# Kernel tuning notes

Measured on AMD Instinct MI355X. Metric: run time of the kernel, lower is better.

The kernel has to match this reference:

```python
import jax, jax.numpy as jnp
import numpy as np

N, E, F_IN = 100000, 3200000, 512
H1, D1, C = 8, 8, 16  # layer1 heads, per-head dim; layer2 out classes
NEG_SLOPE = 0.2


def _segment_softmax(e, dst, num_segments):
    # numerically-stable softmax over edges grouped by destination node
    m = jax.ops.segment_max(e, dst, num_segments=num_segments)
    ex = jnp.exp(e - m[dst])
    s = jax.ops.segment_sum(ex, dst, num_segments=num_segments)
    return ex / (s[dst] + 1e-16)


def _gat_layer(x, src, dst, W, a_src, a_dst, heads, d_out):
    n = x.shape[0]
    h = (x @ W).reshape(n, heads, d_out)          # [N,H,D]
    al_s = jnp.einsum('nhd,hd->nh', h, a_src)     # [N,H]
    al_d = jnp.einsum('nhd,hd->nh', h, a_dst)
    e = jax.nn.leaky_relu(al_s[src] + al_d[dst], NEG_SLOPE)  # [E,H]
    alpha = _segment_softmax(e, dst, n)           # [E,H]
    msg = h[src] * alpha[..., None]               # [E,H,D]
    return jax.ops.segment_sum(msg, dst, num_segments=n)  # [N,H,D]


def setup_inputs() -> dict:
    key = jax.random.key(0)
    ks = jax.random.split(key, 8)
    x = jax.random.normal(ks[0], (N, F_IN), dtype=jnp.float32)
    edge_index = jax.random.randint(ks[1], (2, E), 0, N, dtype=jnp.int64)
    W1 = jax.random.normal(ks[2], (F_IN, H1 * D1), dtype=jnp.float32) * (1.0 / np.sqrt(F_IN))
    a1_src = jax.random.normal(ks[3], (H1, D1), dtype=jnp.float32)
    a1_dst = jax.random.normal(ks[4], (H1, D1), dtype=jnp.float32)
    W2 = jax.random.normal(ks[5], (H1 * D1, C), dtype=jnp.float32) * (1.0 / np.sqrt(H1 * D1))
    a2_src = jax.random.normal(ks[6], (1, C), dtype=jnp.float32)
    a2_dst = jax.random.normal(ks[7], (1, C), dtype=jnp.float32)
    return {'x': x, 'edge_index': edge_index, 'W1': W1, 'a1_src': a1_src,
            'a1_dst': a1_dst, 'W2': W2, 'a2_src': a2_src, 'a2_dst': a2_dst}


def reference(x, edge_index, W1, a1_src, a1_dst, W2, a2_src, a2_dst):
    src, dst = edge_index[0], edge_index[1]
    # layer 1: 8 heads, concat, then ELU (dropout is identity in eval mode)
    h1 = _gat_layer(x, src, dst, W1, a1_src, a1_dst, H1, D1)  # [N,H1,D1]
    h1 = jax.nn.elu(h1.reshape(N, H1 * D1))                   # [N,64]
    # layer 2: single head -> class logits
    h2 = _gat_layer(h1, src, dst, W2, a2_src, a2_dst, 1, C)   # [N,1,C]
    return jax.nn.log_softmax(h2.reshape(N, C), axis=1)
```

## Files before the change

### kernel.cpp

```cpp
#include <hip/hip_runtime.h>
#include <math.h>

#define NEG 0.2f
#define NB 64
#define BCAP 128
#define WS 544

typedef __attribute__((ext_vector_type(8))) short bf16x8;
typedef __attribute__((ext_vector_type(4))) float f32x4;
typedef unsigned long long ull;

#define GL4(dst, ptr) asm volatile("global_load_dwordx4 %0, %1, off" : "=v"(dst) : "v"(ptr))

static __device__ __forceinline__ float lrelu(float x){ return x > 0.f ? x : NEG*x; }

static __device__ __forceinline__ void bsplit(float v, unsigned int& hi, unsigned int& lo){
  unsigned int u = __float_as_uint(v);
  unsigned int hb = (u + 0x7fffu + ((u >> 16) & 1u)) & 0xffff0000u;
  float hf = __uint_as_float(hb);
  float l = v - hf;
  unsigned int ul = __float_as_uint(l);
  hi = hb >> 16;
  lo = (ul + 0x7fffu + ((ul >> 16) & 1u)) >> 16;
}

static __device__ __forceinline__ float bf2f(unsigned short u){
  return __uint_as_float(((unsigned int)u) << 16);
}
static __device__ __forceinline__ unsigned short f2bf(float v){
  unsigned int u = __float_as_uint(v);
  return (unsigned short)((u + 0x7fffu + ((u >> 16) & 1u)) >> 16);
}

static __device__ __forceinline__ bf16x8 cvt8(f32x4 v0, f32x4 v1){
  bf16x8 r;
  #pragma unroll
  for (int i = 0; i < 4; ++i) r[i] = (short)f2bf(v0[i]);
  #pragma unroll
  for (int i = 0; i < 4; ++i) r[4+i] = (short)f2bf(v1[i]);
  return r;
}

__global__ void k_prep(const int* __restrict__ u, int* __restrict__ flag,
                       int* __restrict__ pcur, const float* __restrict__ W1,
                       unsigned short* __restrict__ wtH, unsigned short* __restrict__ wtL){
  int t = blockIdx.x*256 + threadIdx.x;
  if (t < NB*8*16) pcur[t] = 0;
  else if (t < NB*8*16 + 512*64) {
    int i = t - NB*8*16;
    int c = i & 63;
    unsigned int hi, lo;
    bsplit(W1[i], hi, lo);
    wtH[c*WS + (i >> 6)] = (unsigned short)hi;
    wtL[c*WS + (i >> 6)] = (unsigned short)lo;
  } else if (t == NB*8*16 + 512*64) {
    int z = 1;
    for (int e = 0; e < 64; ++e) if (u[2*e+1] != 0) { z = 0; break; }
    *flag = z;
  }
}

__global__ __launch_bounds__(256) void k_part(const int* __restrict__ u,
    const int* __restrict__ flag, int* __restrict__ pcur,
    ull* __restrict__ part, int E, int n, int SEGCAP){
  __shared__ ull buf[NB][BCAP];
  __shared__ int bcnt[NB];
  __shared__ int binc[NB];
  __shared__ int bbase;
  __shared__ int nflush;
  __shared__ unsigned char flist[NB];
  const bool f = (*flag) != 0;
  const int tid = threadIdx.x;
  const int g = blockIdx.x & 7;
  if (tid < NB) bcnt[tid] = 0;
  const long long stride = (long long)gridDim.x * 256;
  const long long iters = ((long long)E + stride - 1) / stride;
  long long e = (long long)blockIdx.x*256 + tid;
  for (long long it = 0; it < iters; ++it, e += stride) {
    if (tid < NB) binc[tid] = 0;
    if (tid == 0) nflush = 0;
    __syncthreads();
    int src = 0, dst = 0, b = 0;
    const bool valid = (e < E);
    if (valid) {
      src = f ? u[2*e] : u[e];
      dst = f ? u[2*(E+e)] : u[E+e];
      b = (int)(((long long)dst * NB) / n);
      atomicAdd(&binc[b], 1);
    }
    __syncthreads();
    if (tid < NB && bcnt[tid] > 0 && bcnt[tid] + binc[tid] > BCAP) {
      int i = atomicAdd(&nflush, 1);
      flist[i] = (unsigned char)tid;
    }
    __syncthreads();
    for (int i = 0; i < nflush; ++i) {
      int b2 = flist[i];
      int c = bcnt[b2]; if (c > BCAP) c = BCAP;
      if (tid == 0) bbase = atomicAdd(&pcur[(b2*8+g)*16], c);
      __syncthreads();
      int base = bbase;
      for (int j = tid; j < c; j += 256) {
        int pos = base + j;
        if (pos < SEGCAP) part[(size_t)(b2*8+g)*SEGCAP + pos] = buf[b2][j];
      }
      __syncthreads();
      if (tid == 0) bcnt[b2] = 0;
      __syncthreads();
    }
    if (valid) {
      int pos = atomicAdd(&bcnt[b], 1);
      if (pos < BCAP) buf[b][pos] = (ull)(unsigned)src | ((ull)(unsigned)dst << 32);
    }
    __syncthreads();
  }
  for (int b2 = 0; b2 < NB; ++b2) {
    int c = bcnt[b2]; if (c > BCAP) c = BCAP;
    if (c > 0) {
      if (tid == 0) bbase = atomicAdd(&pcur[(b2*8+g)*16], c);
      __syncthreads();
      int base = bbase;
      for (int j = tid; j < c; j += 256) {
        int pos = base + j;
        if (pos < SEGCAP) part[(size_t)(b2*8+g)*SEGCAP + pos] = buf[b2][j];
      }
    }
    __syncthreads();
  }
}

__global__ __launch_bounds__(1024) void k_histL(const int* __restrict__ pcur,
    const ull* __restrict__ part, int* __restrict__ cnt, int n, int SEGCAP){
  __shared__ int lcnt[1664];
  const int b = blockIdx.x;
  const int lo = (int)(((long long)b * n + NB - 1) / NB);
  const int hi = (int)(((long long)(b+1) * n + NB - 1) / NB);
  const int m = hi - lo;
  for (int i = threadIdx.x; i < m; i += 1024) lcnt[i] = 0;
  __syncthreads();
  for (int g = 0; g < 8; ++g) {
    int s = b*8 + g;
    int c = pcur[s*16]; if (c > SEGCAP) c = SEGCAP;
    for (int i = threadIdx.x; i < c; i += 1024) {
      ull v = __builtin_nontemporal_load(&part[(size_t)s*SEGCAP + i]);
      atomicAdd(&lcnt[(int)(unsigned)(v >> 32) - lo], 1);
    }
  }
  __syncthreads();
  for (int i = threadIdx.x; i < m; i += 1024) cnt[lo + i] = lcnt[i];
}

__global__ __launch_bounds__(256) void k_scan1(const int* __restrict__ cnt,
    int* __restrict__ ro, int* __restrict__ bsum, int n){
  int t = threadIdx.x;
  int base = blockIdx.x*1024 + t*4;
  int v0 = (base+0 < n) ? cnt[base+0] : 0;
  int v1 = (base+1 < n) ? cnt[base+1] : 0;
  int v2 = (base+2 < n) ? cnt[base+2] : 0;
  int v3 = (base+3 < n) ? cnt[base+3] : 0;
  int s = v0+v1+v2+v3;
  int lane = t & 63, w = t >> 6;
  int inc = s;
  for (int off = 1; off < 64; off <<= 1) {
    int tm = __shfl_up(inc, off);
    if (lane >= off) inc += tm;
  }
  __shared__ int wsum[4];
  if (lane == 63) wsum[w] = inc;
  __syncthreads();
  int wpre = 0;
  for (int k = 0; k < 4; ++k) if (k < w) wpre += wsum[k];
  int run = wpre + inc - s;
  if (base+0 < n) ro[base+0] = run; run += v0;
  if (base+1 < n) ro[base+1] = run; run += v1;
  if (base+2 < n) ro[base+2] = run; run += v2;
  if (base+3 < n) ro[base+3] = run; run += v3;
  if (t == 255) bsum[blockIdx.x] = run;
}

__global__ void k_scan2(int* __restrict__ bsum, int nb){
  int lane = threadIdx.x;
  int carry = 0;
  for (int b = 0; b < nb; b += 64) {
    int i = b + lane;
    int v = (i < nb) ? bsum[i] : 0;
    int inc = v;
    for (int off = 1; off < 64; off <<= 1) {
      int t = __shfl_up(inc, off);
      if (lane >= off) inc += t;
    }
    if (i < nb) bsum[i] = carry + inc - v;
    carry += __shfl(inc, 63);
  }
}

__global__ void k_scan3(int* __restrict__ ro, const int* __restrict__ bsum,
                        int* __restrict__ csr, int n, int E){
  int i = blockIdx.x*blockDim.x + threadIdx.x;
  if (i < n) ro[i] = ro[i] + bsum[i >> 10];
  if (i == 0) ro[n] = E;
  if (i < 16) csr[E + i] = 0;
}

__global__ __launch_bounds__(1024) void k_fillL(const int* __restrict__ pcur,
    const ull* __restrict__ part, const int* __restrict__ ro,
    int* __restrict__ csr, int n, int SEGCAP){
  __shared__ int lcur[1664];
  const int b = blockIdx.x;
  const int lo = (int)(((long long)b * n + NB - 1) / NB);
  const int hi = (int)(((long long)(b+1) * n + NB - 1) / NB);
  const int m = hi - lo;
  for (int i = threadIdx.x; i < m; i += 1024) lcur[i] = ro[lo + i];
  __syncthreads();
  for (int g = 0; g < 8; ++g) {
    int s = b*8 + g;
    int c = pcur[s*16]; if (c > SEGCAP) c = SEGCAP;
    for (int i = threadIdx.x; i < c; i += 1024) {
      ull v = __builtin_nontemporal_load(&part[(size_t)s*SEGCAP + i]);
      int src = (int)(unsigned)v;
      int dst = (int)(unsigned)(v >> 32);
      int p = atomicAdd(&lcur[dst - lo], 1);
      csr[p] = src;
    }
  }
}

__global__ __launch_bounds__(256, 3) void k_proj1(const float* __restrict__ x,
    const unsigned short* __restrict__ wtH, const unsigned short* __restrict__ wtL,
    const float* __restrict__ a1s_g, const float* __restrict__ a1d_g,
    unsigned short* __restrict__ h1bf, float* __restrict__ al1s, float* __restrict__ al1d, int n){
  const int tid = threadIdx.x;
  const int lane = tid & 63;
  const int w = tid >> 6;
  const int l16 = lane & 15;
  const int lhi = lane >> 4;
  const int r0 = blockIdx.x*128 + w*32;

  float as_c[4], ad_c[4];
  #pragma unroll
  for (int f = 0; f < 4; ++f) { as_c[f] = a1s_g[16*f + l16]; ad_c[f] = a1d_g[16*f + l16]; }

  f32x4 acc[2][4];
  #pragma unroll
  for (int m = 0; m < 2; ++m)
    #pragma unroll
    for (int f = 0; f < 4; ++f) acc[m][f] = (f32x4){0.f,0.f,0.f,0.f};

  int rowA = r0 + l16;        if (rowA >= n) rowA = n - 1;
  int rowB = r0 + 16 + l16;   if (rowB >= n) rowB = n - 1;
  const float* xA = x + (size_t)rowA*512 + 8*lhi;
  const float* xB = x + (size_t)rowB*512 + 8*lhi;
  const unsigned short* wHp = wtH + (size_t)l16*WS + 8*lhi;
  const unsigned short* wLp = wtL + (size_t)l16*WS + 8*lhi;

  for (int k0 = 0; k0 < 512; k0 += 64) {
    f32x4 a0, a1v, a2, a3, b0, b1v, b2, b3;
    bf16x8 bh0[4], bl0[4], bh1[4], bl1[4];
    GL4(a0,  xA + k0);      GL4(a1v, xA + k0 + 4);
    GL4(a2,  xA + k0 + 32); GL4(a3,  xA + k0 + 36);
    GL4(b0,  xB + k0);      GL4(b1v, xB + k0 + 4);
    GL4(b2,  xB + k0 + 32); GL4(b3,  xB + k0 + 36);
    #pragma unroll
    for (int f = 0; f < 4; ++f) {
      GL4(bh0[f], wHp + (size_t)f*16*WS + k0);
      GL4(bl0[f], wLp + (size_t)f*16*WS + k0);
      GL4(bh1[f], wHp + (size_t)f*16*WS + k0 + 32);
      GL4(bl1[f], wLp + (size_t)f*16*WS + k0 + 32);
    }
    asm volatile("s_waitcnt vmcnt(0)" ::: "memory");
    __builtin_amdgcn_sched_barrier(0);
    bf16x8 ahA0 = cvt8(a0, a1v), ahA1 = cvt8(a2, a3);
    bf16x8 ahB0 = cvt8(b0, b1v), ahB1 = cvt8(b2, b3);
    #pragma unroll
    for (int f = 0; f < 4; ++f) {
      acc[0][f] = __builtin_amdgcn_mfma_f32_16x16x32_bf16(ahA0, bh0[f], acc[0][f], 0, 0, 0);
      acc[0][f] = __builtin_amdgcn_mfma_f32_16x16x32_bf16(ahA0, bl0[f], acc[0][f], 0, 0, 0);
      acc[0][f] = __builtin_amdgcn_mfma_f32_16x16x32_bf16(ahA1, bh1[f], acc[0][f], 0, 0, 0);
      acc[0][f] = __builtin_amdgcn_mfma_f32_16x16x32_bf16(ahA1, bl1[f], acc[0][f], 0, 0, 0);
      acc[1][f] = __builtin_amdgcn_mfma_f32_16x16x32_bf16(ahB0, bh0[f], acc[1][f], 0, 0, 0);
      acc[1][f] = __builtin_amdgcn_mfma_f32_16x16x32_bf16(ahB0, bl0[f], acc[1][f], 0, 0, 0);
      acc[1][f] = __builtin_amdgcn_mfma_f32_16x16x32_bf16(ahB1, bh1[f], acc[1][f], 0, 0, 0);
      acc[1][f] = __builtin_amdgcn_mfma_f32_16x16x32_bf16(ahB1, bl1[f], acc[1][f], 0, 0, 0);
    }
  }

  #pragma unroll
  for (int m = 0; m < 2; ++m) {
    #pragma unroll
    for (int r = 0; r < 4; ++r) {
      int node = r0 + 16*m + 4*lhi + r;
      bool ok = (node < n);
      #pragma unroll
      for (int f = 0; f < 4; ++f) {
        float v = acc[m][f][r];
        if (ok) h1bf[(size_t)node*64 + 16*f + l16] = f2bf(v);
        float vs = v * as_c[f], vd = v * ad_c[f];
        vs += __shfl_xor(vs, 1); vs += __shfl_xor(vs, 2); vs += __shfl_xor(vs, 4);
        vd += __shfl_xor(vd, 1); vd += __shfl_xor(vd, 2); vd += __shfl_xor(vd, 4);
        if (ok && (l16 & 7) == 0) {
          int head = 2*f + (l16 >> 3);
          al1s[node*8 + head] = vs;
          al1d[node*8 + head] = vd;
        }
      }
    }
  }
}

__global__ __launch_bounds__(256) void k_agg1(const int* __restrict__ ro,
    const int* __restrict__ csr, const float* __restrict__ al1s,
    const float* __restrict__ al1d, const unsigned short* __restrict__ h1bf,
    float* __restrict__ h1b, int n){
  int wid = blockIdx.x*4 + (threadIdx.x >> 6);
  if (wid >= n) return;
  int node = __builtin_amdgcn_readfirstlane(wid);
  int lane = threadIdx.x & 63;
  int half = lane >> 5;
  int sl = lane & 31;
  int h = sl >> 2;
  int beg = ro[node], end = ro[node+1];
  float ald = al1d[node*8 + h];
  float s = 0.f, accA = 0.f, accB = 0.f;
  if (beg < end) {
    int srcb[4]; float alb[4]; unsigned hvb[4];
    #pragma unroll
    for (int j = 0; j < 4; ++j) srcb[j] = csr[beg + 2*j + half];
    #pragma unroll
    for (int j = 0; j < 4; ++j) {
      alb[j] = al1s[srcb[j]*8 + h];
      hvb[j] = *(const unsigned*)&h1bf[(size_t)srcb[j]*64 + 2*sl];
    }
    for (int t = beg; t < end; t += 8) {
      int nsrc[4]; float nal[4]; unsigned nhv[4];
      #pragma unroll
      for (int j = 0; j < 4; ++j) nsrc[j] = csr[t + 8 + 2*j + half];
      #pragma unroll
      for (int j = 0; j < 4; ++j) {
        nal[j] = al1s[nsrc[j]*8 + h];
        nhv[j] = *(const unsigned*)&h1bf[(size_t)nsrc[j]*64 + 2*sl];
      }
      #pragma unroll
      for (int j = 0; j < 4; ++j) {
        float e = alb[j] + ald;
        e = e > 0.f ? e : NEG*e;
        float ex = (t + 2*j + half < end) ? __expf(e) : 0.f;
        s += ex;
        unsigned u = hvb[j];
        accA = fmaf(__uint_as_float(u << 16), ex, accA);
        accB = fmaf(__uint_as_float(u & 0xffff0000u), ex, accB);
      }
      #pragma unroll
      for (int j = 0; j < 4; ++j) { srcb[j] = nsrc[j]; alb[j] = nal[j]; hvb[j] = nhv[j]; }
    }
  }
  s    += __shfl_xor(s, 32);
  accA += __shfl_xor(accA, 32);
  accB += __shfl_xor(accB, 32);
  if (half == 0) {
    float inv = 1.f / (s + 1e-16f);
    float vA = accA * inv, vB = accB * inv;
    vA = vA > 0.f ? vA : expm1f(vA);
    vB = vB > 0.f ? vB : expm1f(vB);
    *(float2*)&h1b[(size_t)node*64 + 2*sl] = make_float2(vA, vB);
  }
}

__global__ __launch_bounds__(256) void k_proj2(const float* __restrict__ h1b,
    const float* __restrict__ W2, const float* __restrict__ a2s_g, const float* __restrict__ a2d_g,
    unsigned short* __restrict__ h2bf, float* __restrict__ al2s, float* __restrict__ al2d, int n){
  __shared__ float w[64*16];
  __shared__ float a2sv[16], a2dv[16];
  for (int i = threadIdx.x; i < 1024; i += 256) w[i] = W2[i];
  if (threadIdx.x < 16) { a2sv[threadIdx.x] = a2s_g[threadIdx.x]; a2dv[threadIdx.x] = a2d_g[threadIdx.x]; }
  __syncthreads();
  int c = threadIdx.x & 15;
  int nid = blockIdx.x*16 + (threadIdx.x >> 4);
  if (nid >= n) return;
  const float* row = h1b + (size_t)nid*64;
  float acc = 0.f;
  #pragma unroll
  for (int k0 = 0; k0 < 64; k0 += 4) {
    float4 r = *(const float4*)(row + k0);
    acc = fmaf(r.x, w[(k0+0)*16 + c], acc);
    acc = fmaf(r.y, w[(k0+1)*16 + c], acc);
    acc = fmaf(r.z, w[(k0+2)*16 + c], acc);
    acc = fmaf(r.w, w[(k0+3)*16 + c], acc);
  }
  h2bf[(size_t)nid*16 + c] = f2bf(acc);
  float vs = acc * a2sv[c], vd = acc * a2dv[c];
  vs += __shfl_xor(vs, 1); vs += __shfl_xor(vs, 2); vs += __shfl_xor(vs, 4); vs += __shfl_xor(vs, 8);
  vd += __shfl_xor(vd, 1); vd += __shfl_xor(vd, 2); vd += __shfl_xor(vd, 4); vd += __shfl_xor(vd, 8);
  if (c == 0) { al2s[nid] = vs; al2d[nid] = vd; }
}

__global__ __launch_bounds__(256) void k_agg2(const int* __restrict__ ro,
    const int* __restrict__ csr, const float* __restrict__ al2s,
    const float* __restrict__ al2d, const unsigned short* __restrict__ h2bf,
    float* __restrict__ out, int n){
  int wid = blockIdx.x*4 + (threadIdx.x >> 6);
  if (wid >= n) return;
  int node = __builtin_amdgcn_readfirstlane(wid);
  int lane = threadIdx.x & 63;
  int j = lane >> 4, c = lane & 15;
  int beg = ro[node], end = ro[node+1];
  float ald = al2d[node];
  float sp = 0.f, acc = 0.f;
  if (beg < end) {
    int iA = beg + j;
    int sA = csr[iA];
    int sB = csr[iA + 4];
    float aA = al2s[sA];
    float hA = bf2f(h2bf[(size_t)sA*16 + c]);
    float aB = al2s[sB];
    float hB = bf2f(h2bf[(size_t)sB*16 + c]);
    for (int i = iA; i < end; i += 4) {
      int sC = csr[i + 8];
      float aC = al2s[sC];
      float hC = bf2f(h2bf[(size_t)sC*16 + c]);
      float e = lrelu(aA + ald);
      float ex = __expf(e);
      sp += ex;
      acc = fmaf(ex, hA, acc);
      aA = aB; hA = hB; aB = aC; hB = hC;
    }
  }
  sp  += __shfl_xor(sp, 16);  sp  += __shfl_xor(sp, 32);
  acc += __shfl_xor(acc, 16); acc += __shfl_xor(acc, 32);
  float v = acc / (sp + 1e-16f);
  float mx = v;
  mx = fmaxf(mx, __shfl_xor(mx, 1)); mx = fmaxf(mx, __shfl_xor(mx, 2));
  mx = fmaxf(mx, __shfl_xor(mx, 4)); mx = fmaxf(mx, __shfl_xor(mx, 8));
  float l = v - mx;
  float se = __expf(l);
  se += __shfl_xor(se, 1); se += __shfl_xor(se, 2);
  se += __shfl_xor(se, 4); se += __shfl_xor(se, 8);
  float res = l - logf(se);
  if (j == 0) out[(size_t)node*16 + c] = res;
}

static inline size_t alignup(size_t x){ return (x + 255) & ~(size_t)255; }

extern "C" void kernel_launch(void* const* d_in, const int* in_sizes, int n_in,
                              void* d_out, int out_size, void* d_ws, size_t ws_size,
                              hipStream_t stream){
  const float* x   = (const float*)d_in[0];
  const int*   ei  = (const int*)  d_in[1];
  const float* W1  = (const float*)d_in[2];
  const float* a1s = (const float*)d_in[3];
  const float* a1d = (const float*)d_in[4];
  const float* W2  = (const float*)d_in[5];
  const float* a2s = (const float*)d_in[6];
  const float* a2d = (const float*)d_in[7];
  float* out = (float*)d_out;

  const int n = in_sizes[0] / 512;
  const int E = in_sizes[1] / 2;

  char* w = (char*)d_ws;
  unsigned short* h1bf = (unsigned short*)w; w += alignup((size_t)n*64*2);
  float* h1b  = (float*)w; w += alignup((size_t)n*64*4);
  float* al1s_ = (float*)w; w += alignup((size_t)n*8*4);
  float* al1d_ = (float*)w; w += alignup((size_t)n*8*4);
  unsigned short* h2bf = (unsigned short*)w; w += alignup((size_t)n*16*2);
  float* al2s_ = (float*)w; w += alignup((size_t)n*4);
  float* al2d_ = (float*)w; w += alignup((size_t)n*4);
  int* cnt    = (int*)w;   w += alignup((size_t)n*4);
  int* ro     = (int*)w;   w += alignup((size_t)(n+1)*4);
  int* csr    = (int*)w;   w += alignup((size_t)(E+16)*4);
  int* bsum   = (int*)w;   w += alignup(512*4);
  int* flag   = (int*)w;   w += alignup(64);
  int* pcur   = (int*)w;   w += alignup((size_t)NB*8*16*4);
  unsigned short* wtH = (unsigned short*)w; w += alignup((size_t)64*WS*2);
  unsigned short* wtL = (unsigned short*)w; w += alignup((size_t)64*WS*2);

  ull* part = (ull*)h1bf;
  const int SEGCAP = 9300;

  const int nb_scan = (n + 1023) / 1024;
  const int prep_threads = NB*8*16 + 512*64 + 1;

  k_prep<<<(prep_threads + 255)/256, 256, 0, stream>>>(ei, flag, pcur, W1, wtH, wtL);
  k_part<<<1024, 256, 0, stream>>>(ei, flag, pcur, part, E, n, SEGCAP);
  k_histL<<<NB, 1024, 0, stream>>>(pcur, part, cnt, n, SEGCAP);
  k_scan1<<<nb_scan, 256, 0, stream>>>(cnt, ro, bsum, n);
  k_scan2<<<1, 64, 0, stream>>>(bsum, nb_scan);
  k_scan3<<<(n+255)/256, 256, 0, stream>>>(ro, bsum, csr, n, E);
  k_fillL<<<NB, 1024, 0, stream>>>(pcur, part, ro, csr, n, SEGCAP);

  k_proj1<<<(n+127)/128, 256, 0, stream>>>(x, wtH, wtL, a1s, a1d, h1bf, al1s_, al1d_, n);
  k_agg1<<<(n+3)/4, 256, 0, stream>>>(ro, csr, al1s_, al1d_, h1bf, h1b, n);
  k_proj2<<<(n+15)/16, 256, 0, stream>>>(h1b, W2, a2s, a2d, h2bf, al2s_, al2d_, n);
  k_agg2<<<(n+3)/4, 256, 0, stream>>>(ro, csr, al2s_, al2d_, h2bf, out, n);
}
```

Baseline: 484.5 us.

## Fuse edge partitioning and layer-1 projection into one concurrent kernel launch

Merges the edge bucketing kernel and the layer-1 MFMA projection into a single launch, with the first 1024 blocks partitioning edges and the rest computing x@W1. Partitioning is atomic/latency bound and the projection streams x through the MFMA units, so running them side by side is meant to overlap the two phases and drop one launch. The partition buffer no longer aliases h1bf, so it gets its own ~38MB of workspace. Launch bounds drop to 2 blocks/CU because of the shared-memory buffer, which may reduce occupancy for the projection blocks.

```diff
diff --git a/kernel.cpp b/kernel.cpp
--- a/kernel.cpp
+++ b/kernel.cpp
@@ -5,6 +5,7 @@
 #define NB 64
 #define BCAP 128
 #define WS 544
+#define NPART 1024
 
 typedef __attribute__((ext_vector_type(8))) short bf16x8;
 typedef __attribute__((ext_vector_type(4))) float f32x4;
@@ -60,72 +61,157 @@
   }
 }
 
-__global__ __launch_bounds__(256) void k_part(const int* __restrict__ u,
-    const int* __restrict__ flag, int* __restrict__ pcur,
-    ull* __restrict__ part, int E, int n, int SEGCAP){
+__global__ __launch_bounds__(256, 2) void k_p1p(
+    const int* __restrict__ u, const int* __restrict__ flag,
+    int* __restrict__ pcur, ull* __restrict__ part, int E, int n, int SEGCAP,
+    const float* __restrict__ x,
+    const unsigned short* __restrict__ wtH, const unsigned short* __restrict__ wtL,
+    const float* __restrict__ a1s_g, const float* __restrict__ a1d_g,
+    unsigned short* __restrict__ h1bf, float* __restrict__ al1s, float* __restrict__ al1d){
   __shared__ ull buf[NB][BCAP];
   __shared__ int bcnt[NB];
   __shared__ int binc[NB];
   __shared__ int bbase;
   __shared__ int nflush;
   __shared__ unsigned char flist[NB];
-  const bool f = (*flag) != 0;
+
+  if (blockIdx.x < NPART) {
+    const bool f = (*flag) != 0;
+    const int tid = threadIdx.x;
+    const int g = blockIdx.x & 7;
+    if (tid < NB) bcnt[tid] = 0;
+    const long long stride = (long long)NPART * 256;
+    const long long iters = ((long long)E + stride - 1) / stride;
+    long long e = (long long)blockIdx.x*256 + tid;
+    for (long long it = 0; it < iters; ++it, e += stride) {
+      if (tid < NB) binc[tid] = 0;
+      if (tid == 0) nflush = 0;
+      __syncthreads();
+      int src = 0, dst = 0, b = 0;
+      const bool valid = (e < E);
+      if (valid) {
+        src = f ? u[2*e] : u[e];
+        dst = f ? u[2*(E+e)] : u[E+e];
+        b = (int)(((long long)dst * NB) / n);
+        atomicAdd(&binc[b], 1);
+      }
+      __syncthreads();
+      if (tid < NB && bcnt[tid] > 0 && bcnt[tid] + binc[tid] > BCAP) {
+        int i = atomicAdd(&nflush, 1);
+        flist[i] = (unsigned char)tid;
+      }
+      __syncthreads();
+      for (int i = 0; i < nflush; ++i) {
+        int b2 = flist[i];
+        int c = bcnt[b2]; if (c > BCAP) c = BCAP;
+        if (tid == 0) bbase = atomicAdd(&pcur[(b2*8+g)*16], c);
+        __syncthreads();
+        int base = bbase;
+        for (int j = tid; j < c; j += 256) {
+          int pos = base + j;
+          if (pos < SEGCAP) part[(size_t)(b2*8+g)*SEGCAP + pos] = buf[b2][j];
+        }
+        __syncthreads();
+        if (tid == 0) bcnt[b2] = 0;
+        __syncthreads();
+      }
+      if (valid) {
+        int pos = atomicAdd(&bcnt[b], 1);
+        if (pos < BCAP) buf[b][pos] = (ull)(unsigned)src | ((ull)(unsigned)dst << 32);
+      }
+      __syncthreads();
+    }
+    for (int b2 = 0; b2 < NB; ++b2) {
+      int c = bcnt[b2]; if (c > BCAP) c = BCAP;
+      if (c > 0) {
+        if (tid == 0) bbase = atomicAdd(&pcur[(b2*8+g)*16], c);
+        __syncthreads();
+        int base = bbase;
+        for (int j = tid; j < c; j += 256) {
+          int pos = base + j;
+          if (pos < SEGCAP) part[(size_t)(b2*8+g)*SEGCAP + pos] = buf[b2][j];
+        }
+      }
+      __syncthreads();
+    }
+    return;
+  }
+
   const int tid = threadIdx.x;
-  const int g = blockIdx.x & 7;
-  if (tid < NB) bcnt[tid] = 0;
-  const long long stride = (long long)gridDim.x * 256;
-  const long long iters = ((long long)E + stride - 1) / stride;
-  long long e = (long long)blockIdx.x*256 + tid;
-  for (long long it = 0; it < iters; ++it, e += stride) {
-    if (tid < NB) binc[tid] = 0;
-    if (tid == 0) nflush = 0;
-    __syncthreads();
-    int src = 0, dst = 0, b = 0;
-    const bool valid = (e < E);
-    if (valid) {
-      src = f ? u[2*e] : u[e];
-      dst = f ? u[2*(E+e)] : u[E+e];
-      b = (int)(((long long)dst * NB) / n);
-      atomicAdd(&binc[b], 1);
-    }
-    __syncthreads();
-    if (tid < NB && bcnt[tid] > 0 && bcnt[tid] + binc[tid] > BCAP) {
-      int i = atomicAdd(&nflush, 1);
-      flist[i] = (unsigned char)tid;
-    }
-    __syncthreads();
-    for (int i = 0; i < nflush; ++i) {
-      int b2 = flist[i];
-      int c = bcnt[b2]; if (c > BCAP) c = BCAP;
-      if (tid == 0) bbase = atomicAdd(&pcur[(b2*8+g)*16], c);
-      __syncthreads();
-      int base = bbase;
-      for (int j = tid; j < c; j += 256) {
-        int pos = base + j;
-        if (pos < SEGCAP) part[(size_t)(b2*8+g)*SEGCAP + pos] = buf[b2][j];
-      }
-      __syncthreads();
-      if (tid == 0) bcnt[b2] = 0;
-      __syncthreads();
-    }
-    if (valid) {
-      int pos = atomicAdd(&bcnt[b], 1);
-      if (pos < BCAP) buf[b][pos] = (ull)(unsigned)src | ((ull)(unsigned)dst << 32);
-    }
-    __syncthreads();
-  }
-  for (int b2 = 0; b2 < NB; ++b2) {
-    int c = bcnt[b2]; if (c > BCAP) c = BCAP;
-    if (c > 0) {
-      if (tid == 0) bbase = atomicAdd(&pcur[(b2*8+g)*16], c);
-      __syncthreads();
-      int base = bbase;
-      for (int j = tid; j < c; j += 256) {
-        int pos = base + j;
-        if (pos < SEGCAP) part[(size_t)(b2*8+g)*SEGCAP + pos] = buf[b2][j];
-      }
-    }
-    __syncthreads();
+  const int lane = tid & 63;
+  const int w = tid >> 6;
+  const int l16 = lane & 15;
+  const int lhi = lane >> 4;
+  const int r0 = (blockIdx.x - NPART)*128 + w*32;
+
+  float as_c[4], ad_c[4];
+  #pragma unroll
+  for (int f = 0; f < 4; ++f) { as_c[f] = a1s_g[16*f + l16]; ad_c[f] = a1d_g[16*f + l16]; }
+
+  f32x4 acc[2][4];
+  #pragma unroll
+  for (int m = 0; m < 2; ++m)
+    #pragma unroll
+    for (int f = 0; f < 4; ++f) acc[m][f] = (f32x4){0.f,0.f,0.f,0.f};
+
+  int rowA = r0 + l16;        if (rowA >= n) rowA = n - 1;
+  int rowB = r0 + 16 + l16;   if (rowB >= n) rowB = n - 1;
+  const float* xA = x + (size_t)rowA*512 + 8*lhi;
+  const float* xB = x + (size_t)rowB*512 + 8*lhi;
+  const unsigned short* wHp = wtH + (size_t)l16*WS + 8*lhi;
+  const unsigned short* wLp = wtL + (size_t)l16*WS + 8*lhi;
+
+  for (int k0 = 0; k0 < 512; k0 += 64) {
+    f32x4 a0, a1v, a2, a3, b0, b1v, b2, b3;
+    bf16x8 bh0[4], bl0[4], bh1[4], bl1[4];
+    GL4(a0,  xA + k0);      GL4(a1v, xA + k0 + 4);
+    GL4(a2,  xA + k0 + 32); GL4(a3,  xA + k0 + 36);
+    GL4(b0,  xB + k0);      GL4(b1v, xB + k0 + 4);
+    GL4(b2,  xB + k0 + 32); GL4(b3,  xB + k0 + 36);
+    #pragma unroll
+    for (int f = 0; f < 4; ++f) {
+      GL4(bh0[f], wHp + (size_t)f*16*WS + k0);
+      GL4(bl0[f], wLp + (size_t)f*16*WS + k0);
+      GL4(bh1[f], wHp + (size_t)f*16*WS + k0 + 32);
+      GL4(bl1[f], wLp + (size_t)f*16*WS + k0 + 32);
+    }
+    asm volatile("s_waitcnt vmcnt(0)" ::: "memory");
+    __builtin_amdgcn_sched_barrier(0);
+    bf16x8 ahA0 = cvt8(a0, a1v), ahA1 = cvt8(a2, a3);
+    bf16x8 ahB0 = cvt8(b0, b1v), ahB1 = cvt8(b2, b3);
+    #pragma unroll
+    for (int f = 0; f < 4; ++f) {
+      acc[0][f] = __builtin_amdgcn_mfma_f32_16x16x32_bf16(ahA0, bh0[f], acc[0][f], 0, 0, 0);
+      acc[0][f] = __builtin_amdgcn_mfma_f32_16x16x32_bf16(ahA0, bl0[f], acc[0][f], 0, 0, 0);
+      acc[0][f] = __builtin_amdgcn_mfma_f32_16x16x32_bf16(ahA1, bh1[f], acc[0][f], 0, 0, 0);
+      acc[0][f] = __builtin_amdgcn_mfma_f32_16x16x32_bf16(ahA1, bl1[f], acc[0][f], 0, 0, 0);
+      acc[1][f] = __builtin_amdgcn_mfma_f32_16x16x32_bf16(ahB0, bh0[f], acc[1][f], 0, 0, 0);
+      acc[1][f] = __builtin_amdgcn_mfma_f32_16x16x32_bf16(ahB0, bl0[f], acc[1][f], 0, 0, 0);
+      acc[1][f] = __builtin_amdgcn_mfma_f32_16x16x32_bf16(ahB1, bh1[f], acc[1][f], 0, 0, 0);
+      acc[1][f] = __builtin_amdgcn_mfma_f32_16x16x32_bf16(ahB1, bl1[f], acc[1][f], 0, 0, 0);
+    }
+  }
+
+  #pragma unroll
+  for (int m = 0; m < 2; ++m) {
+    #pragma unroll
+    for (int r = 0; r < 4; ++r) {
+      int node = r0 + 16*m + 4*lhi + r;
+      bool ok = (node < n);
+      #pragma unroll
+      for (int f = 0; f < 4; ++f) {
+        float v = acc[m][f][r];
+        if (ok) h1bf[(size_t)node*64 + 16*f + l16] = f2bf(v);
+        float vs = v * as_c[f], vd = v * ad_c[f];
+        vs += __shfl_xor(vs, 1); vs += __shfl_xor(vs, 2); vs += __shfl_xor(vs, 4);
+        vd += __shfl_xor(vd, 1); vd += __shfl_xor(vd, 2); vd += __shfl_xor(vd, 4);
+        if (ok && (l16 & 7) == 0) {
+          int head = 2*f + (l16 >> 3);
+          al1s[node*8 + head] = vs;
+          al1d[node*8 + head] = vd;
+        }
+      }
+    }
   }
 }
 
@@ -225,88 +311,6 @@
   }
 }
 
-__global__ __launch_bounds__(256, 3) void k_proj1(const float* __restrict__ x,
-    const unsigned short* __restrict__ wtH, const unsigned short* __restrict__ wtL,
-    const float* __restrict__ a1s_g, const float* __restrict__ a1d_g,
-    unsigned short* __restrict__ h1bf, float* __restrict__ al1s, float* __restrict__ al1d, int n){
-  const int tid = threadIdx.x;
-  const int lane = tid & 63;
-  const int w = tid >> 6;
-  const int l16 = lane & 15;
-  const int lhi = lane >> 4;
-  const int r0 = blockIdx.x*128 + w*32;
-
-  float as_c[4], ad_c[4];
-  #pragma unroll
-  for (int f = 0; f < 4; ++f) { as_c[f] = a1s_g[16*f + l16]; ad_c[f] = a1d_g[16*f + l16]; }
-
-  f32x4 acc[2][4];
-  #pragma unroll
-  for (int m = 0; m < 2; ++m)
-    #pragma unroll
-    for (int f = 0; f < 4; ++f) acc[m][f] = (f32x4){0.f,0.f,0.f,0.f};
-
-  int rowA = r0 + l16;        if (rowA >= n) rowA = n - 1;
-  int rowB = r0 + 16 + l16;   if (rowB >= n) rowB = n - 1;
-  const float* xA = x + (size_t)rowA*512 + 8*lhi;
-  const float* xB = x + (size_t)rowB*512 + 8*lhi;
-  const unsigned short* wHp = wtH + (size_t)l16*WS + 8*lhi;
-  const unsigned short* wLp = wtL + (size_t)l16*WS + 8*lhi;
-
-  for (int k0 = 0; k0 < 512; k0 += 64) {
-    f32x4 a0, a1v, a2, a3, b0, b1v, b2, b3;
-    bf16x8 bh0[4], bl0[4], bh1[4], bl1[4];
-    GL4(a0,  xA + k0);      GL4(a1v, xA + k0 + 4);
-    GL4(a2,  xA + k0 + 32); GL4(a3,  xA + k0 + 36);
-    GL4(b0,  xB + k0);      GL4(b1v, xB + k0 + 4);
-    GL4(b2,  xB + k0 + 32); GL4(b3,  xB + k0 + 36);
-    #pragma unroll
-    for (int f = 0; f < 4; ++f) {
-      GL4(bh0[f], wHp + (size_t)f*16*WS + k0);
-      GL4(bl0[f], wLp + (size_t)f*16*WS + k0);
-      GL4(bh1[f], wHp + (size_t)f*16*WS + k0 + 32);
-      GL4(bl1[f], wLp + (size_t)f*16*WS + k0 + 32);
-    }
-    asm volatile("s_waitcnt vmcnt(0)" ::: "memory");
-    __builtin_amdgcn_sched_barrier(0);
-    bf16x8 ahA0 = cvt8(a0, a1v), ahA1 = cvt8(a2, a3);
-    bf16x8 ahB0 = cvt8(b0, b1v), ahB1 = cvt8(b2, b3);
-    #pragma unroll
-    for (int f = 0; f < 4; ++f) {
-      acc[0][f] = __builtin_amdgcn_mfma_f32_16x16x32_bf16(ahA0, bh0[f], acc[0][f], 0, 0, 0);
-      acc[0][f] = __builtin_amdgcn_mfma_f32_16x16x32_bf16(ahA0, bl0[f], acc[0][f], 0, 0, 0);
-      acc[0][f] = __builtin_amdgcn_mfma_f32_16x16x32_bf16(ahA1, bh1[f], acc[0][f], 0, 0, 0);
-      acc[0][f] = __builtin_amdgcn_mfma_f32_16x16x32_bf16(ahA1, bl1[f], acc[0][f], 0, 0, 0);
-      acc[1][f] = __builtin_amdgcn_mfma_f32_16x16x32_bf16(ahB0, bh0[f], acc[1][f], 0, 0, 0);
-      acc[1][f] = __builtin_amdgcn_mfma_f32_16x16x32_bf16(ahB0, bl0[f], acc[1][f], 0, 0, 0);
-      acc[1][f] = __builtin_amdgcn_mfma_f32_16x16x32_bf16(ahB1, bh1[f], acc[1][f], 0, 0, 0);
-      acc[1][f] = __builtin_amdgcn_mfma_f32_16x16x32_bf16(ahB1, bl1[f], acc[1][f], 0, 0, 0);
-    }
-  }
-
-  #pragma unroll
-  for (int m = 0; m < 2; ++m) {
-    #pragma unroll
-    for (int r = 0; r < 4; ++r) {
-      int node = r0 + 16*m + 4*lhi + r;
-      bool ok = (node < n);
-      #pragma unroll
-      for (int f = 0; f < 4; ++f) {
-        float v = acc[m][f][r];
-        if (ok) h1bf[(size_t)node*64 + 16*f + l16] = f2bf(v);
-        float vs = v * as_c[f], vd = v * ad_c[f];
-        vs += __shfl_xor(vs, 1); vs += __shfl_xor(vs, 2); vs += __shfl_xor(vs, 4);
-        vd += __shfl_xor(vd, 1); vd += __shfl_xor(vd, 2); vd += __shfl_xor(vd, 4);
-        if (ok && (l16 & 7) == 0) {
-          int head = 2*f + (l16 >> 3);
-          al1s[node*8 + head] = vs;
-          al1d[node*8 + head] = vd;
-        }
-      }
-    }
-  }
-}
-
 __global__ __launch_bounds__(256) void k_agg1(const int* __restrict__ ro,
     const int* __restrict__ csr, const float* __restrict__ al1s,
     const float* __restrict__ al1d, const unsigned short* __restrict__ h1bf,
@@ -345,9 +349,9 @@
         e = e > 0.f ? e : NEG*e;
         float ex = (t + 2*j + half < end) ? __expf(e) : 0.f;
         s += ex;
-        unsigned u = hvb[j];
-        accA = fmaf(__uint_as_float(u << 16), ex, accA);
-        accB = fmaf(__uint_as_float(u & 0xffff0000u), ex, accB);
+        unsigned u0 = hvb[j];
+        accA = fmaf(__uint_as_float(u0 << 16), ex, accA);
+        accB = fmaf(__uint_as_float(u0 & 0xffff0000u), ex, accB);
       }
       #pragma unroll
       for (int j = 0; j < 4; ++j) { srcb[j] = nsrc[j]; alb[j] = nal[j]; hvb[j] = nhv[j]; }
@@ -473,21 +477,22 @@
   unsigned short* wtH = (unsigned short*)w; w += alignup((size_t)64*WS*2);
   unsigned short* wtL = (unsigned short*)w; w += alignup((size_t)64*WS*2);
 
-  ull* part = (ull*)h1bf;
+  ull* part = (ull*)w; w += alignup((size_t)512*9300*8);
   const int SEGCAP = 9300;
 
   const int nb_scan = (n + 1023) / 1024;
   const int prep_threads = NB*8*16 + 512*64 + 1;
+  const int nproj = (n + 127) / 128;
 
   k_prep<<<(prep_threads + 255)/256, 256, 0, stream>>>(ei, flag, pcur, W1, wtH, wtL);
-  k_part<<<1024, 256, 0, stream>>>(ei, flag, pcur, part, E, n, SEGCAP);
+  k_p1p<<<NPART + nproj, 256, 0, stream>>>(ei, flag, pcur, part, E, n, SEGCAP,
+                                           x, wtH, wtL, a1s, a1d, h1bf, al1s_, al1d_);
   k_histL<<<NB, 1024, 0, stream>>>(pcur, part, cnt, n, SEGCAP);
   k_scan1<<<nb_scan, 256, 0, stream>>>(cnt, ro, bsum, n);
   k_scan2<<<1, 64, 0, stream>>>(bsum, nb_scan);
   k_scan3<<<(n+255)/256, 256, 0, stream>>>(ro, bsum, csr, n, E);
   k_fillL<<<NB, 1024, 0, stream>>>(pcur, part, ro, csr, n, SEGCAP);
 
-  k_proj1<<<(n+127)/128, 256, 0, stream>>>(x, wtH, wtL, a1s, a1d, h1bf, al1s_, al1d_, n);
   k_agg1<<<(n+3)/4, 256, 0, stream>>>(ro, csr, al1s_, al1d_, h1bf, h1b, n);
   k_proj2<<<(n+15)/16, 256, 0, stream>>>(h1b, W2, a2s, a2d, h2bf, al2s_, al2d_, n);
   k_agg2<<<(n+3)/4, 256, 0, stream>>>(ro, csr, al2s_, al2d_, h2bf, out, n);
```

Result: slower. 504.6 us (+4.1%).
